# Performance work log

Hardware: AMD Instinct MI355X
Metric: run time of the kernel (lower is better)

## Reference

```python
import jax, jax.numpy as jnp
import numpy as np
from jax import lax

H = 20  # hidden_size


def _rnn_layer(x_seq, h0, W_ih, W_hh, b_ih, b_hh):
    """Vanilla tanh RNN layer. x_seq: [B,T,D], h0: [B,H]. Returns ([B,T,H], [B,H])."""
    # Precompute input projection for all timesteps (the only large GEMM).
    xp = jnp.einsum('btd,hd->bth', x_seq, W_ih) + b_ih + b_hh  # [B,T,H]

    def step(h, xt):
        h = jnp.tanh(xt + h @ W_hh.T)
        return h, h

    h_last, hs = lax.scan(step, h0, jnp.swapaxes(xp, 0, 1))  # hs: [T,B,H]
    return jnp.swapaxes(hs, 0, 1), h_last


def setup_inputs() -> dict:
    key = jax.random.key(0)
    ks = jax.random.split(key, 12)
    B, T = 4096, 512
    s = 1.0 / np.sqrt(H)  # PyTorch default uniform(-1/sqrt(H), 1/sqrt(H))
    u = lambda k, shape: jax.random.uniform(k, shape, jnp.float32, -s, s)
    return {
        'x': jax.random.normal(ks[0], (B, T, 1), jnp.float32),
        'hidden': jax.random.normal(ks[1], (2, B, H), jnp.float32),
        'W_ih0': u(ks[2], (H, 1)),
        'W_hh0': u(ks[3], (H, H)),
        'b_ih0': u(ks[4], (H,)),
        'b_hh0': u(ks[5], (H,)),
        'W_ih1': u(ks[6], (H, H)),
        'W_hh1': u(ks[7], (H, H)),
        'b_ih1': u(ks[8], (H,)),
        'b_hh1': u(ks[9], (H,)),
        'fc_w': u(ks[10], (1, H)),
        'fc_b': u(ks[11], (1,)),
    }


def reference(x, hidden, W_ih0, W_hh0, b_ih0, b_hh0, W_ih1, W_hh1, b_ih1, b_hh1, fc_w, fc_b):
    # 2-layer vanilla RNN (eval mode: inter-layer dropout disabled)
    h0_seq, h0_last = _rnn_layer(x, hidden[0], W_ih0, W_hh0, b_ih0, b_hh0)
    h1_seq, h1_last = _rnn_layer(h0_seq, hidden[1], W_ih1, W_hh1, b_ih1, b_hh1)
    out = h1_seq[:, -1, :] @ fc_w.T + fc_b  # [B,1]
    new_hidden = jnp.stack([h0_last, h1_last], axis=0)  # [2,B,H]
    return out, new_hidden
```

## Files before the change

kernel.cpp:

```cpp
#include <hip/hip_runtime.h>


#define Bsz 4096
#define Tn  512
#define Hn  20
#define GB  8
#define K   8
#define RING 16
#define NPH (Tn / K)
#define XPAD 516
#define NTHREADS 128

typedef float v2 __attribute__((ext_vector_type(2)));

__device__ __forceinline__ float tanh_fast(float v) {
    float e = __expf(2.0f * v);
    return 1.0f - 2.0f * __builtin_amdgcn_rcpf(e + 1.0f);
}

#define DOT20P(acc, accb, W, H) do { \
    acc  = __builtin_elementwise_fma(W##0, H##0, acc);  \
    accb = __builtin_elementwise_fma(W##1, H##1, accb); \
    acc  = __builtin_elementwise_fma(W##2, H##2, acc);  \
    accb = __builtin_elementwise_fma(W##3, H##3, accb); \
    acc  = __builtin_elementwise_fma(W##4, H##4, acc);  \
    accb = __builtin_elementwise_fma(W##5, H##5, accb); \
    acc  = __builtin_elementwise_fma(W##6, H##6, acc);  \
    accb = __builtin_elementwise_fma(W##7, H##7, accb); \
    acc  = __builtin_elementwise_fma(W##8, H##8, acc);  \
    accb = __builtin_elementwise_fma(W##9, H##9, accb); \
} while (0)

#define LOAD_ROWP(W, ptr) \
    v2 W##0, W##1, W##2, W##3, W##4, W##5, W##6, W##7, W##8, W##9; \
    { const float4* _p = (const float4*)(ptr); \
      float4 _t; \
      _t = _p[0]; W##0 = (v2){_t.x, _t.y}; W##1 = (v2){_t.z, _t.w}; \
      _t = _p[1]; W##2 = (v2){_t.x, _t.y}; W##3 = (v2){_t.z, _t.w}; \
      _t = _p[2]; W##4 = (v2){_t.x, _t.y}; W##5 = (v2){_t.z, _t.w}; \
      _t = _p[3]; W##6 = (v2){_t.x, _t.y}; W##7 = (v2){_t.z, _t.w}; \
      _t = _p[4]; W##8 = (v2){_t.x, _t.y}; W##9 = (v2){_t.z, _t.w}; }

#define READ_H(H, base) \
    v2 H##0, H##1, H##2, H##3, H##4, H##5, H##6, H##7, H##8, H##9; \
    { const float4 _a = *(const float4*)((base) + 0);  \
      const float4 _b = *(const float4*)((base) + 4);  \
      const float4 _c = *(const float4*)((base) + 8);  \
      const float4 _d = *(const float4*)((base) + 12); \
      const float4 _e = *(const float4*)((base) + 16); \
      H##0 = (v2){_a.x, _a.y}; H##1 = (v2){_a.z, _a.w}; \
      H##2 = (v2){_b.x, _b.y}; H##3 = (v2){_b.z, _b.w}; \
      H##4 = (v2){_c.x, _c.y}; H##5 = (v2){_c.z, _c.w}; \
      H##6 = (v2){_d.x, _d.y}; H##7 = (v2){_d.z, _d.w}; \
      H##8 = (v2){_e.x, _e.y}; H##9 = (v2){_e.z, _e.w}; }

__global__ __launch_bounds__(NTHREADS)
__attribute__((amdgpu_waves_per_eu(1, 1)))
void rnn2_fused(const float* __restrict__ x,
                const float* __restrict__ hidden,
                const float* __restrict__ W_ih0,
                const float* __restrict__ W_hh0,
                const float* __restrict__ b_ih0,
                const float* __restrict__ b_hh0,
                const float* __restrict__ W_ih1,
                const float* __restrict__ W_hh1,
                const float* __restrict__ b_ih1,
                const float* __restrict__ b_hh1,
                const float* __restrict__ fc_w,
                const float* __restrict__ fc_b,
                float* __restrict__ out)
{
    const int tid  = threadIdx.x;
    const int wave = tid >> 6;
    const int lane = tid & 63;
    const int g    = lane >> 3;
    const int jj   = lane & 7;
    const int r0   = jj;
    const int r1   = jj + 8;
    const int r2   = (jj + 16 < Hn) ? (jj + 16) : (Hn - 1);
    const int b    = blockIdx.x * GB + g;

    __shared__ float xs[GB][XPAD];
    __shared__ float h0r[RING][GB][Hn];
    __shared__ float h1s[GB][Hn];

    const float* mA = (wave == 0) ? W_hh0 : W_ih1;
    LOAD_ROWP(wA0, mA + r0 * Hn)
    LOAD_ROWP(wA1, mA + r1 * Hn)
    LOAD_ROWP(wA2, mA + r2 * Hn)
    LOAD_ROWP(wB0, W_hh1 + r0 * Hn)
    LOAD_ROWP(wB1, W_hh1 + r1 * Hn)
    LOAD_ROWP(wB2, W_hh1 + r2 * Hn)

    const float wih0_0 = W_ih0[r0], wih0_1 = W_ih0[r1], wih0_2 = W_ih0[r2];
    const float bA0 = (wave == 0) ? (b_ih0[r0] + b_hh0[r0]) : (b_ih1[r0] + b_hh1[r0]);
    const float bA1 = (wave == 0) ? (b_ih0[r1] + b_hh0[r1]) : (b_ih1[r1] + b_hh1[r1]);
    const float bA2 = (wave == 0) ? (b_ih0[r2] + b_hh0[r2]) : (b_ih1[r2] + b_hh1[r2]);

    {
        const int bB = blockIdx.x * GB;
        #pragma unroll
        for (int r = 0; r < (GB * Tn) / (NTHREADS * 4); ++r) {
            const int c  = (r * NTHREADS + tid) * 4;
            const int gg = c >> 9;
            const int t  = c & (Tn - 1);
            float4 v = *(const float4*)(x + (long)(bB + gg) * Tn + t);
            *(float4*)&xs[gg][t] = v;
        }
    }

    if (wave == 0) {
        h0r[RING - 1][g][r0] = hidden[(long)b * Hn + r0];
        h0r[RING - 1][g][r1] = hidden[(long)b * Hn + r1];
        h0r[RING - 1][g][r2] = hidden[(long)b * Hn + r2];
    } else {
        h1s[g][r0] = hidden[(long)Bsz * Hn + (long)b * Hn + r0];
        h1s[g][r1] = hidden[(long)Bsz * Hn + (long)b * Hn + r1];
        h1s[g][r2] = hidden[(long)Bsz * Hn + (long)b * Hn + r2];
    }
    __syncthreads();

    float k0 = 0.f, k1 = 0.f, k2 = 0.f;

    for (int k = 0; k <= NPH; ++k) {
        if (wave == 0) {
            if (k < NPH) {
                #pragma unroll
                for (int u = 0; u < K; ++u) {
                    const int t = k * K + u;
                    READ_H(hA, &h0r[(t - 1) & (RING - 1)][g][0])
                    const float xt = xs[g][t];
                    v2 a0 = (v2){fmaf(xt, wih0_0, bA0), 0.f}, a0b = (v2){0.f, 0.f};
                    v2 a1 = (v2){fmaf(xt, wih0_1, bA1), 0.f}, a1b = (v2){0.f, 0.f};
                    v2 a2 = (v2){fmaf(xt, wih0_2, bA2), 0.f}, a2b = (v2){0.f, 0.f};
                    DOT20P(a0, a0b, wA0, hA);
                    DOT20P(a1, a1b, wA1, hA);
                    DOT20P(a2, a2b, wA2, hA);
                    const v2 s0 = a0 + a0b, s1 = a1 + a1b, s2 = a2 + a2b;
                    k0 = tanh_fast(s0.x + s0.y);
                    k1 = tanh_fast(s1.x + s1.y);
                    k2 = tanh_fast(s2.x + s2.y);
                    const int q = t & (RING - 1);
                    h0r[q][g][r0] = k0;
                    h0r[q][g][r1] = k1;
                    h0r[q][g][r2] = k2;
                }
            }
        } else {
            if (k > 0) {
                #pragma unroll
                for (int u = 0; u < K; ++u) {
                    const int t = (k - 1) * K + u;
                    READ_H(hA, &h0r[t & (RING - 1)][g][0])
                    READ_H(hB, &h1s[g][0])
                    v2 a0 = (v2){bA0, 0.f}, a0b = (v2){0.f, 0.f};
                    v2 a1 = (v2){bA1, 0.f}, a1b = (v2){0.f, 0.f};
                    v2 a2 = (v2){bA2, 0.f}, a2b = (v2){0.f, 0.f};
                    v2 c0 = (v2){0.f, 0.f}, c0b = (v2){0.f, 0.f};
                    v2 c1 = (v2){0.f, 0.f}, c1b = (v2){0.f, 0.f};
                    v2 c2 = (v2){0.f, 0.f}, c2b = (v2){0.f, 0.f};
                    DOT20P(a0, a0b, wA0, hA);
                    DOT20P(a1, a1b, wA1, hA);
                    DOT20P(a2, a2b, wA2, hA);
                    DOT20P(c0, c0b, wB0, hB);
                    DOT20P(c1, c1b, wB1, hB);
                    DOT20P(c2, c2b, wB2, hB);
                    const v2 s0 = (a0 + a0b) + (c0 + c0b);
                    const v2 s1 = (a1 + a1b) + (c1 + c1b);
                    const v2 s2 = (a2 + a2b) + (c2 + c2b);
                    k0 = tanh_fast(s0.x + s0.y);
                    k1 = tanh_fast(s1.x + s1.y);
                    k2 = tanh_fast(s2.x + s2.y);
                    h1s[g][r0] = k0;
                    h1s[g][r1] = k1;
                    h1s[g][r2] = k2;
                }
            }
        }
        if (k < NPH) __syncthreads();
    }

    if (wave == 0) {
        out[Bsz + (long)b * Hn + r0] = k0;
        out[Bsz + (long)b * Hn + r1] = k1;
        out[Bsz + (long)b * Hn + r2] = k2;
    } else {
        out[Bsz + (long)Bsz * Hn + (long)b * Hn + r0] = k0;
        out[Bsz + (long)Bsz * Hn + (long)b * Hn + r1] = k1;
        out[Bsz + (long)Bsz * Hn + (long)b * Hn + r2] = k2;
        if (jj == 0) {
            LOAD_ROWP(fw, fc_w)
            READ_H(hv, &h1s[g][0])
            v2 aA = (v2){fc_b[0], 0.f};
            v2 aB = (v2){0.f, 0.f};
            DOT20P(aA, aB, fw, hv);
            const v2 s = aA + aB;
            out[b] = s.x + s.y;
        }
    }
}

extern "C" void kernel_launch(void* const* d_in, const int* in_sizes, int n_in,
                              void* d_out, int out_size, void* d_ws, size_t ws_size,
                              hipStream_t stream) {
    const float* x      = (const float*)d_in[0];
    const float* hidden = (const float*)d_in[1];
    const float* W_ih0  = (const float*)d_in[2];
    const float* W_hh0  = (const float*)d_in[3];
    const float* b_ih0  = (const float*)d_in[4];
    const float* b_hh0  = (const float*)d_in[5];
    const float* W_ih1  = (const float*)d_in[6];
    const float* W_hh1  = (const float*)d_in[7];
    const float* b_ih1  = (const float*)d_in[8];
    const float* b_hh1  = (const float*)d_in[9];
    const float* fc_w   = (const float*)d_in[10];
    const float* fc_b   = (const float*)d_in[11];

    rnn2_fused<<<Bsz / GB, NTHREADS, 0, stream>>>(
        x, hidden, W_ih0, W_hh0, b_ih0, b_hh0,
        W_ih1, W_hh1, b_ih1, b_hh1, fc_w, fc_b, (float*)d_out);
}
```

Measured before the change: 127.7 us.

## Move layer-1 input projection into layer-0 wave to balance the two waves

Wave 0 now computes both the layer-0 recurrence and the layer-1 input projection W_ih1·h0 for each step, writing the projected values into a 32-deep shared ring. Wave 1 then only runs the layer-1 recurrent dot product plus tanh, with the pipeline lag extended by one phase. This evens out the FMA work between the two waves, since wave 1 previously did twice the dot products and set the critical path. The cost is one extra phase and barrier, a larger shared buffer, and more work on wave 0's own serial dependency chain.

Result: slower. 144.0 us (+12.7%).

```diff
diff --git a/kernel.cpp b/kernel.cpp
--- a/kernel.cpp
+++ b/kernel.cpp
@@ -6,7 +6,7 @@
 #define Hn  20
 #define GB  8
 #define K   8
-#define RING 16
+#define ZR  32
 #define NPH (Tn / K)
 #define XPAD 516
 #define NTHREADS 128
@@ -81,21 +81,25 @@
     const int b    = blockIdx.x * GB + g;
 
     __shared__ float xs[GB][XPAD];
-    __shared__ float h0r[RING][GB][Hn];
+    __shared__ float zr[ZR][GB][Hn];
+    __shared__ float h0s[GB][Hn];
     __shared__ float h1s[GB][Hn];
 
-    const float* mA = (wave == 0) ? W_hh0 : W_ih1;
-    LOAD_ROWP(wA0, mA + r0 * Hn)
-    LOAD_ROWP(wA1, mA + r1 * Hn)
-    LOAD_ROWP(wA2, mA + r2 * Hn)
-    LOAD_ROWP(wB0, W_hh1 + r0 * Hn)
-    LOAD_ROWP(wB1, W_hh1 + r1 * Hn)
-    LOAD_ROWP(wB2, W_hh1 + r2 * Hn)
+    const float* mZ = (wave == 0) ? W_ih1 : W_hh1;
+    LOAD_ROWP(wA0, W_hh0 + r0 * Hn)
+    LOAD_ROWP(wA1, W_hh0 + r1 * Hn)
+    LOAD_ROWP(wA2, W_hh0 + r2 * Hn)
+    LOAD_ROWP(wZ0, mZ + r0 * Hn)
+    LOAD_ROWP(wZ1, mZ + r1 * Hn)
+    LOAD_ROWP(wZ2, mZ + r2 * Hn)
 
     const float wih0_0 = W_ih0[r0], wih0_1 = W_ih0[r1], wih0_2 = W_ih0[r2];
-    const float bA0 = (wave == 0) ? (b_ih0[r0] + b_hh0[r0]) : (b_ih1[r0] + b_hh1[r0]);
-    const float bA1 = (wave == 0) ? (b_ih0[r1] + b_hh0[r1]) : (b_ih1[r1] + b_hh1[r1]);
-    const float bA2 = (wave == 0) ? (b_ih0[r2] + b_hh0[r2]) : (b_ih1[r2] + b_hh1[r2]);
+    const float bA0 = b_ih0[r0] + b_hh0[r0];
+    const float bA1 = b_ih0[r1] + b_hh0[r1];
+    const float bA2 = b_ih0[r2] + b_hh0[r2];
+    const float bZ0 = b_ih1[r0] + b_hh1[r0];
+    const float bZ1 = b_ih1[r1] + b_hh1[r1];
+    const float bZ2 = b_ih1[r2] + b_hh1[r2];
 
     {
         const int bB = blockIdx.x * GB;
@@ -110,9 +114,9 @@
     }
 
     if (wave == 0) {
-        h0r[RING - 1][g][r0] = hidden[(long)b * Hn + r0];
-        h0r[RING - 1][g][r1] = hidden[(long)b * Hn + r1];
-        h0r[RING - 1][g][r2] = hidden[(long)b * Hn + r2];
+        h0s[g][r0] = hidden[(long)b * Hn + r0];
+        h0s[g][r1] = hidden[(long)b * Hn + r1];
+        h0s[g][r2] = hidden[(long)b * Hn + r2];
     } else {
         h1s[g][r0] = hidden[(long)Bsz * Hn + (long)b * Hn + r0];
         h1s[g][r1] = hidden[(long)Bsz * Hn + (long)b * Hn + r1];
@@ -122,62 +126,80 @@
 
     float k0 = 0.f, k1 = 0.f, k2 = 0.f;
 
-    for (int k = 0; k <= NPH; ++k) {
+    for (int k = 0; k <= NPH + 1; ++k) {
         if (wave == 0) {
             if (k < NPH) {
                 #pragma unroll
                 for (int u = 0; u < K; ++u) {
                     const int t = k * K + u;
-                    READ_H(hA, &h0r[(t - 1) & (RING - 1)][g][0])
+                    READ_H(hA, &h0s[g][0])
                     const float xt = xs[g][t];
                     v2 a0 = (v2){fmaf(xt, wih0_0, bA0), 0.f}, a0b = (v2){0.f, 0.f};
                     v2 a1 = (v2){fmaf(xt, wih0_1, bA1), 0.f}, a1b = (v2){0.f, 0.f};
                     v2 a2 = (v2){fmaf(xt, wih0_2, bA2), 0.f}, a2b = (v2){0.f, 0.f};
+                    v2 z0 = (v2){bZ0, 0.f}, z0b = (v2){0.f, 0.f};
+                    v2 z1 = (v2){bZ1, 0.f}, z1b = (v2){0.f, 0.f};
+                    v2 z2 = (v2){bZ2, 0.f}, z2b = (v2){0.f, 0.f};
                     DOT20P(a0, a0b, wA0, hA);
                     DOT20P(a1, a1b, wA1, hA);
                     DOT20P(a2, a2b, wA2, hA);
+                    DOT20P(z0, z0b, wZ0, hA);
+                    DOT20P(z1, z1b, wZ1, hA);
+                    DOT20P(z2, z2b, wZ2, hA);
                     const v2 s0 = a0 + a0b, s1 = a1 + a1b, s2 = a2 + a2b;
                     k0 = tanh_fast(s0.x + s0.y);
                     k1 = tanh_fast(s1.x + s1.y);
                     k2 = tanh_fast(s2.x + s2.y);
-                    const int q = t & (RING - 1);
-                    h0r[q][g][r0] = k0;
-                    h0r[q][g][r1] = k1;
-                    h0r[q][g][r2] = k2;
+                    h0s[g][r0] = k0;
+                    h0s[g][r1] = k1;
+                    h0s[g][r2] = k2;
+                    const v2 t0 = z0 + z0b, t1 = z1 + z1b, t2 = z2 + z2b;
+                    const int zq = (t - 1) & (ZR - 1);
+                    zr[zq][g][r0] = t0.x + t0.y;
+                    zr[zq][g][r1] = t1.x + t1.y;
+                    zr[zq][g][r2] = t2.x + t2.y;
                 }
+            } else if (k == NPH) {
+                READ_H(hA, &h0s[g][0])
+                v2 z0 = (v2){bZ0, 0.f}, z0b = (v2){0.f, 0.f};
+                v2 z1 = (v2){bZ1, 0.f}, z1b = (v2){0.f, 0.f};
+                v2 z2 = (v2){bZ2, 0.f}, z2b = (v2){0.f, 0.f};
+                DOT20P(z0, z0b, wZ0, hA);
+                DOT20P(z1, z1b, wZ1, hA);
+                DOT20P(z2, z2b, wZ2, hA);
+                const v2 t0 = z0 + z0b, t1 = z1 + z1b, t2 = z2 + z2b;
+                const int zq = (Tn - 1) & (ZR - 1);
+                zr[zq][g][r0] = t0.x + t0.y;
+                zr[zq][g][r1] = t1.x + t1.y;
+                zr[zq][g][r2] = t2.x + t2.y;
             }
         } else {
-            if (k > 0) {
+            if (k >= 2) {
                 #pragma unroll
                 for (int u = 0; u < K; ++u) {
-                    const int t = (k - 1) * K + u;
-                    READ_H(hA, &h0r[t & (RING - 1)][g][0])
+                    const int t = (k - 2) * K + u;
+                    const int zq = t & (ZR - 1);
+                    const float zv0 = zr[zq][g][r0];
+                    const float zv1 = zr[zq][g][r1];
+                    const float zv2 = zr[zq][g][r2];
                     READ_H(hB, &h1s[g][0])
-                    v2 a0 = (v2){bA0, 0.f}, a0b = (v2){0.f, 0.f};
-                    v2 a1 = (v2){bA1, 0.f}, a1b = (v2){0.f, 0.f};
-                    v2 a2 = (v2){bA2, 0.f}, a2b = (v2){0.f, 0.f};
                     v2 c0 = (v2){0.f, 0.f}, c0b = (v2){0.f, 0.f};
                     v2 c1 = (v2){0.f, 0.f}, c1b = (v2){0.f, 0.f};
                     v2 c2 = (v2){0.f, 0.f}, c2b = (v2){0.f, 0.f};
-                    DOT20P(a0, a0b, wA0, hA);
-                    DOT20P(a1, a1b, wA1, hA);
-                    DOT20P(a2, a2b, wA2, hA);
-                    DOT20P(c0, c0b, wB0, hB);
-                    DOT20P(c1, c1b, wB1, hB);
-                    DOT20P(c2, c2b, wB2, hB);
-                    const v2 s0 = (a0 + a0b) + (c0 + c0b);
-                    const v2 s1 = (a1 + a1b) + (c1 + c1b);
-                    const v2 s2 = (a2 + a2b) + (c2 + c2b);
-                    k0 = tanh_fast(s0.x + s0.y);
-                    k1 = tanh_fast(s1.x + s1.y);
-                    k2 = tanh_fast(s2.x + s2.y);
+                    DOT20P(c0, c0b, wZ0, hB);
+                    DOT20P(c1, c1b, wZ1, hB);
+                    DOT20P(c2, c2b, wZ2, hB);
+                    const v2 s0 = c0 + c0b, s1 = c1 + c1b, s2 = c2 + c2b;
+                    k0 = tanh_fast(zv0 + s0.x + s0.y);
+                    k1 = tanh_fast(zv1 + s1.x + s1.y);
+                    k2 = tanh_fast(zv2 + s2.x + s2.y);
                     h1s[g][r0] = k0;
                     h1s[g][r1] = k1;
                     h1s[g][r2] = k2;
                 }
             }
         }
-        if (k < NPH) __syncthreads();
+        if (k <= NPH) __syncthreads();
     }
 
     if (wave == 0) {
```
